# Performance work log

Measured on AMD Instinct MI355X. Metric: run time of the kernel, lower is better.

The kernel has to match this reference:

```python
import jax, jax.numpy as jnp
import numpy as np

D_MODEL = 1024
D_STATE = 16
EXPAND = 2
D_CONV = 4
D_INNER = EXPAND * D_MODEL          # 2048
DT_RANK = D_MODEL // 16             # 64
B = 2
L = 1024
EPS = 1e-5


def setup_inputs() -> dict:
    key = jax.random.key(0)
    ks = jax.random.split(key, 8)
    s = 0.02
    return {
        "x": jax.random.normal(ks[0], (B, L, D_MODEL), jnp.float32),
        "ln_gamma": jnp.ones((D_MODEL,), jnp.float32),
        "ln_beta": jnp.zeros((D_MODEL,), jnp.float32),
        "in_proj_w": jax.random.normal(ks[1], (2 * D_INNER, D_MODEL), jnp.float32) * s,
        "conv_w": jax.random.normal(ks[2], (D_INNER, 1, D_CONV), jnp.float32) * s,
        "conv_b": jnp.zeros((D_INNER,), jnp.float32),
        "x_proj_w": jax.random.normal(ks[3], (DT_RANK + 2 * D_STATE, D_INNER), jnp.float32) * s,
        "dt_proj_w": jax.random.normal(ks[4], (D_INNER, DT_RANK), jnp.float32) * s,
        "dt_proj_b": jax.random.normal(ks[5], (D_INNER,), jnp.float32) * 0.01,
        "A_log": jnp.log(jnp.tile(jnp.arange(1, D_STATE + 1, dtype=jnp.float32), (D_INNER, 1))),
        "D_skip": jnp.ones((D_INNER,), jnp.float32),
        "out_proj_w": jax.random.normal(ks[6], (D_MODEL, D_INNER), jnp.float32) * s,
    }


def _layernorm(x, g, b):
    mu = jnp.mean(x, axis=-1, keepdims=True)
    var = jnp.mean((x - mu) ** 2, axis=-1, keepdims=True)
    return (x - mu) * jax.lax.rsqrt(var + EPS) * g + b


def _mamba_forward(x, ln_gamma, ln_beta, in_proj_w, conv_w, conv_b,
                   x_proj_w, dt_proj_w, dt_proj_b, A_log, D_skip, out_proj_w):
    residual = x
    xn = _layernorm(x, ln_gamma, ln_beta)

    # in_proj -> split into ssm input u and gate z   (b, l, 2*d_inner)
    xz = jnp.einsum('bld,ed->ble', xn, in_proj_w)
    u, z = jnp.split(xz, 2, axis=-1)

    # causal depthwise conv1d (padding = d_conv-1 on the left, truncated to L)
    uc = jnp.transpose(u, (0, 2, 1))  # (b, d_inner, l)
    uc = jax.lax.conv_general_dilated(
        uc, conv_w, window_strides=(1,), padding=[(D_CONV - 1, 0)],
        feature_group_count=D_INNER,
        dimension_numbers=('NCH', 'OIH', 'NCH'))
    uc = uc + conv_b[None, :, None]
    u = jax.nn.silu(jnp.transpose(uc, (0, 2, 1)))  # (b, l, d_inner)

    # selective SSM
    A = -jnp.exp(A_log)                              # (d_inner, d_state)
    x_dbl = jnp.einsum('bld,ed->ble', u, x_proj_w)   # (b, l, dt_rank+2*n)
    dt, Bm, Cm = jnp.split(x_dbl, [DT_RANK, DT_RANK + D_STATE], axis=-1)
    delta = jax.nn.softplus(jnp.einsum('blr,dr->bld', dt, dt_proj_w) + dt_proj_b)

    def step(h, inputs):
        d_t, B_t, C_t, u_t = inputs            # (b,di) (b,n) (b,n) (b,di)
        dA = jnp.exp(d_t[..., None] * A)       # (b, di, n)
        h = dA * h + (d_t * u_t)[..., None] * B_t[:, None, :]
        y = jnp.einsum('bdn,bn->bd', h, C_t)
        return h, y

    h0 = jnp.zeros((x.shape[0], D_INNER, D_STATE), x.dtype)
    xs = (jnp.moveaxis(delta, 1, 0), jnp.moveaxis(Bm, 1, 0),
          jnp.moveaxis(Cm, 1, 0), jnp.moveaxis(u, 1, 0))
    _, ys = jax.lax.scan(step, h0, xs)
    y = jnp.moveaxis(ys, 0, 1) + u * D_skip     # (b, l, d_inner)

    y = y * jax.nn.silu(z)                      # gated output
    out = jnp.einsum('ble,de->bld', y, out_proj_w)
    # dropout is identity in eval mode
    return out + residual


def reference(x, ln_gamma, ln_beta, in_proj_w, conv_w, conv_b,
              x_proj_w, dt_proj_w, dt_proj_b, A_log, D_skip, out_proj_w):
    return _mamba_forward(x, ln_gamma, ln_beta, in_proj_w, conv_w, conv_b,
                          x_proj_w, dt_proj_w, dt_proj_b, A_log, D_skip, out_proj_w)
```

## Files before the change

### kernel.cpp

```cpp
#include <hip/hip_runtime.h>

#define D_MODEL 1024
#define D_STATE 16
#define D_INNER 2048
#define DT_RANK 64
#define NBATCH 2
#define SEQ_L 1024
#define M_ROWS (NBATCH * SEQ_L)
#define CHUNK 64
#define NCHUNK (SEQ_L / CHUNK)

typedef __bf16 bf16x8 __attribute__((ext_vector_type(8)));
typedef float f32x4 __attribute__((ext_vector_type(4)));
typedef unsigned short u16;
typedef unsigned int u32;
typedef u16 u16x8 __attribute__((ext_vector_type(8)));

__device__ __forceinline__ float bf2f(u16 h) {
    return __uint_as_float(((unsigned)h) << 16);
}
__device__ __forceinline__ u16 f2bf(float f) {
    unsigned u = __float_as_uint(f);
    u += 0x7fff + ((u >> 16) & 1);
    return (u16)(u >> 16);
}

__global__ __launch_bounds__(256) void prep(
    const float* __restrict__ s0, const float* __restrict__ s1,
    const float* __restrict__ s2, const float* __restrict__ s3,
    u16* __restrict__ d0, u16* __restrict__ d1,
    u16* __restrict__ d2, u16* __restrict__ d3,
    const float* __restrict__ x, const float* __restrict__ g,
    const float* __restrict__ b, u16* __restrict__ xn,
    float* __restrict__ xd) {
    int blk = blockIdx.x;
    if (blk < 25856) {
        int idx = blk * 256 + threadIdx.x;
        if (idx < 4194304) {
            d0[idx] = f2bf(s0[idx]);
        } else if (idx < 6291456) {
            int i = idx - 4194304; d1[i] = f2bf(s1[i]);
        } else if (idx < 6488064) {
            int i = idx - 6291456; d2[i] = f2bf(s2[i]);
        } else {
            int i = idx - 6488064; d3[i] = f2bf(s3[i]);
        }
        return;
    }
    if (blk < 26048) {
        int zi = (blk - 25856) * 256 + threadIdx.x;
        ((float4*)xd)[zi] = (float4){0.f, 0.f, 0.f, 0.f};
        return;
    }
    int row = blk - 26048;
    const float4* xr = (const float4*)(x + (size_t)row * D_MODEL);
    float4 v = xr[threadIdx.x];
    float s  = v.x + v.y + v.z + v.w;
    float ss = v.x * v.x + v.y * v.y + v.z * v.z + v.w * v.w;
#pragma unroll
    for (int off = 32; off > 0; off >>= 1) {
        s  += __shfl_down(s,  off, 64);
        ss += __shfl_down(ss, off, 64);
    }
    __shared__ float sh_s[4], sh_ss[4];
    int wid = threadIdx.x >> 6;
    if ((threadIdx.x & 63) == 0) { sh_s[wid] = s; sh_ss[wid] = ss; }
    __syncthreads();
    float mu  = (sh_s[0] + sh_s[1] + sh_s[2] + sh_s[3]) * (1.0f / D_MODEL);
    float var = (sh_ss[0] + sh_ss[1] + sh_ss[2] + sh_ss[3]) * (1.0f / D_MODEL) - mu * mu;
    float rs = rsqrtf(var + 1e-5f);
    int c0 = threadIdx.x * 4;
    float vv[4] = {v.x, v.y, v.z, v.w};
#pragma unroll
    for (int j = 0; j < 4; j++) {
        int c = c0 + j;
        float o = (vv[j] - mu) * rs * g[c] + b[c];
        xn[(size_t)row * D_MODEL + c] = f2bf(o);
    }
}

template <int BM, int BN, int WM, int WN, int MODE>
__global__ __launch_bounds__(256) void gemm_lds(
    const __bf16* __restrict__ A, const __bf16* __restrict__ W,
    int K, int Ksteps, int ldC,
    float* __restrict__ outF, u16* __restrict__ outB) {
    constexpr int WCOLS = BN / (WN * 16);
    __shared__ __bf16 As[BM * 32];
    __shared__ __bf16 Bs[BN * 32];
    int tid  = threadIdx.x;
    int lane = tid & 63;
    int wid  = tid >> 6;
    int l16  = lane & 15;
    int quad = lane >> 4;
    int wr = wid / WCOLS;
    int wc = wid % WCOLS;
    int m0 = blockIdx.y * BM;
    int n0 = blockIdx.x * BN;
    int kbase = blockIdx.z * Ksteps * 32;

    f32x4 acc[WM][WN];
#pragma unroll
    for (int mi = 0; mi < WM; mi++)
#pragma unroll
        for (int nj = 0; nj < WN; nj++)
            acc[mi][nj] = (f32x4){0.f, 0.f, 0.f, 0.f};

    for (int ki = 0; ki < Ksteps; ki++) {
        int k0 = kbase + ki * 32;
        __syncthreads();
#pragma unroll
        for (int i = 0; i < BM / 64; i++) {
            int t   = i * 256 + tid;
            int row = t >> 2;
            int cg  = (t & 3) ^ ((row >> 1) & 3);
            __builtin_amdgcn_global_load_lds(
                (const __attribute__((address_space(1))) u32*)(A + (size_t)(m0 + row) * K + k0 + cg * 8),
                (__attribute__((address_space(3))) u32*)(As + (i * 256 + wid * 64) * 8),
                16, 0, 0);
        }
#pragma unroll
        for (int i = 0; i < BN / 64; i++) {
            int t   = i * 256 + tid;
            int row = t >> 2;
            int cg  = (t & 3) ^ ((row >> 1) & 3);
            __builtin_amdgcn_global_load_lds(
                (const __attribute__((address_space(1))) u32*)(W + (size_t)(n0 + row) * K + k0 + cg * 8),
                (__attribute__((address_space(3))) u32*)(Bs + (i * 256 + wid * 64) * 8),
                16, 0, 0);
        }
        __syncthreads();

        bf16x8 af[WM], bfr[WN];
#pragma unroll
        for (int mi = 0; mi < WM; mi++) {
            int r  = wr * WM * 16 + mi * 16 + l16;
            int cg = quad ^ ((r >> 1) & 3);
            af[mi] = *(const bf16x8*)(As + r * 32 + cg * 8);
        }
#pragma unroll
        for (int nj = 0; nj < WN; nj++) {
            int r  = wc * WN * 16 + nj * 16 + l16;
            int cg = quad ^ ((r >> 1) & 3);
            bfr[nj] = *(const bf16x8*)(Bs + r * 32 + cg * 8);
        }
#pragma unroll
        for (int mi = 0; mi < WM; mi++)
#pragma unroll
            for (int nj = 0; nj < WN; nj++)
                acc[mi][nj] = __builtin_amdgcn_mfma_f32_16x16x32_bf16(
                    af[mi], bfr[nj], acc[mi][nj], 0, 0, 0);
    }

    float* outP = (MODE == 4) ? outF + (size_t)blockIdx.z * M_ROWS * ldC : outF;
#pragma unroll
    for (int mi = 0; mi < WM; mi++) {
#pragma unroll
        for (int nj = 0; nj < WN; nj++) {
            int col = n0 + wc * WN * 16 + nj * 16 + l16;
#pragma unroll
            for (int r = 0; r < 4; r++) {
                int row = m0 + wr * WM * 16 + mi * 16 + quad * 4 + r;
                float v = acc[mi][nj][r];
                if (MODE == 0) {
                    outB[(size_t)row * ldC + col] = f2bf(v);
                } else {
                    outP[(size_t)row * ldC + col] = v;
                }
            }
        }
    }
}

__global__ __launch_bounds__(256) void out_reduce(
    const float* __restrict__ p, const float* __restrict__ x,
    float* __restrict__ out) {
    int idx = blockIdx.x * 256 + threadIdx.x;
    const int N = M_ROWS * D_MODEL;
    float4 a = ((const float4*)p)[idx];
    float4 b = ((const float4*)(p + N))[idx];
    float4 c = ((const float4*)(p + 2 * N))[idx];
    float4 d = ((const float4*)(p + 3 * N))[idx];
    float4 r = ((const float4*)x)[idx];
    float4 o;
    o.x = a.x + b.x + c.x + d.x + r.x;
    o.y = a.y + b.y + c.y + d.y + r.y;
    o.z = a.z + b.z + c.z + d.z + r.z;
    o.w = a.w + b.w + c.w + d.w + r.w;
    ((float4*)out)[idx] = o;
}

__global__ __launch_bounds__(256) void gemm_xp(
    const __bf16* __restrict__ A, const __bf16* __restrict__ W,
    float* __restrict__ outF) {
    const int K = D_INNER, Ksplit = D_INNER / 8, Nw = 96;
    int lane = threadIdx.x & 63;
    int wid  = threadIdx.x >> 6;
    int m0 = blockIdx.y * 64;
    int n0 = blockIdx.x * 64;
    int kc = blockIdx.z;
    int l16  = lane & 15;
    int quad = lane >> 4;
    int mrow = m0 + wid * 16 + l16;

    const __bf16* ap = A + (size_t)mrow * K + kc * Ksplit + quad * 8;
    const __bf16* wp[4];
#pragma unroll
    for (int j = 0; j < 4; j++) {
        int nc = n0 + j * 16 + l16;
        if (nc > Nw - 1) nc = Nw - 1;
        wp[j] = W + (size_t)nc * K + kc * Ksplit + quad * 8;
    }
    f32x4 acc[4];
#pragma unroll
    for (int j = 0; j < 4; j++) acc[j] = (f32x4){0.f, 0.f, 0.f, 0.f};

    for (int k = 0; k < Ksplit; k += 32) {
        bf16x8 a = *(const bf16x8*)ap;
        ap += 32;
#pragma unroll
        for (int j = 0; j < 4; j++) {
            bf16x8 bfr = *(const bf16x8*)wp[j];
            wp[j] += 32;
            acc[j] = __builtin_amdgcn_mfma_f32_16x16x32_bf16(a, bfr, acc[j], 0, 0, 0);
        }
    }
#pragma unroll
    for (int j = 0; j < 4; j++) {
        int col = n0 + j * 16 + l16;
        if (col < Nw) {
#pragma unroll
            for (int r = 0; r < 4; r++) {
                int row = m0 + wid * 16 + quad * 4 + r;
                atomicAdd(outF + (size_t)row * 96 + col, acc[j][r]);
            }
        }
    }
}

__global__ __launch_bounds__(256) void gemm_dt(
    const float* __restrict__ A, const __bf16* __restrict__ W,
    const float* __restrict__ bias, u16* __restrict__ outB16) {
    int lane = threadIdx.x & 63;
    int wid  = threadIdx.x >> 6;
    int m0 = blockIdx.y * 64;
    int n0 = blockIdx.x * 64;
    int l16  = lane & 15;
    int quad = lane >> 4;
    int mrow = m0 + wid * 16 + l16;

    const float* ap = A + (size_t)mrow * 96 + quad * 8;
    const __bf16* wp[4];
#pragma unroll
    for (int j = 0; j < 4; j++) {
        int nc = n0 + j * 16 + l16;
        wp[j] = W + (size_t)nc * DT_RANK + quad * 8;
    }
    f32x4 acc[4];
#pragma unroll
    for (int j = 0; j < 4; j++) acc[j] = (f32x4){0.f, 0.f, 0.f, 0.f};

#pragma unroll
    for (int k = 0; k < DT_RANK; k += 32) {
        float4 v0 = *(const float4*)(ap);
        float4 v1 = *(const float4*)(ap + 4);
        ap += 32;
        u16x8 pk;
        pk[0] = f2bf(v0.x); pk[1] = f2bf(v0.y); pk[2] = f2bf(v0.z); pk[3] = f2bf(v0.w);
        pk[4] = f2bf(v1.x); pk[5] = f2bf(v1.y); pk[6] = f2bf(v1.z); pk[7] = f2bf(v1.w);
        bf16x8 a = __builtin_bit_cast(bf16x8, pk);
#pragma unroll
        for (int j = 0; j < 4; j++) {
            bf16x8 bfr = *(const bf16x8*)wp[j];
            wp[j] += 32;
            acc[j] = __builtin_amdgcn_mfma_f32_16x16x32_bf16(a, bfr, acc[j], 0, 0, 0);
        }
    }
#pragma unroll
    for (int j = 0; j < 4; j++) {
        int col = n0 + j * 16 + l16;
#pragma unroll
        for (int r = 0; r < 4; r++) {
            int row = m0 + wid * 16 + quad * 4 + r;
            float t = acc[j][r] + bias[col];
            float sp = (t > 20.f) ? t : log1pf(__expf(t));
            outB16[(size_t)row * D_INNER + col] = f2bf(sp);
        }
    }
}

__global__ __launch_bounds__(256) void conv_silu(
    const u16* __restrict__ xz, const float* __restrict__ cw,
    const float* __restrict__ cb, u16* __restrict__ uc) {
    int idx = blockIdx.x * 256 + threadIdx.x;
    int d = idx & (D_INNER - 1);
    int m = idx >> 11;
    int t = m & (SEQ_L - 1);
    float s = cb[d];
#pragma unroll
    for (int j = 0; j < 4; j++) {
        int tt = t - 3 + j;
        if (tt >= 0) {
            s += cw[d * 4 + j] *
                 bf2f(xz[(size_t)(m - 3 + j) * (2 * D_INNER) + d]);
        }
    }
    float sig = 1.f / (1.f + __expf(-s));
    uc[idx] = f2bf(s * sig);
}

__global__ __launch_bounds__(256) void scan_chunk(
    const u16* __restrict__ delta, const u16* __restrict__ uc,
    const float* __restrict__ xd, const float* __restrict__ A_log,
    float* __restrict__ Pst, float* __restrict__ Sst) {
    __shared__ float Bsh[CHUNK][16];
    int tid  = threadIdx.x;
    int lane = tid & 63;
    int w    = tid >> 6;
    int dsub = lane & 15;
    int g    = lane >> 4;
    int n0   = g * 4;
    int c = blockIdx.x, b = blockIdx.z;
    int d = blockIdx.y * 64 + w * 16 + dsub;
    int mbase = b * SEQ_L + c * CHUNK;

    {
        int row = tid >> 2, q = tid & 3;
        *(float4*)&Bsh[row][q * 4] =
            *(const float4*)(xd + (size_t)(mbase + row) * 96 + DT_RANK + q * 4);
    }
    __syncthreads();

    float a[4];
    {
        float4 a0 = *(const float4*)(A_log + d * D_STATE + n0);
        a[0] = -__expf(a0.x); a[1] = -__expf(a0.y);
        a[2] = -__expf(a0.z); a[3] = -__expf(a0.w);
    }
    float P[4] = {1.f, 1.f, 1.f, 1.f}, S[4] = {0.f, 0.f, 0.f, 0.f};

    for (int t0 = 0; t0 < CHUNK; t0 += 4) {
        float dlv[4], uv[4];
#pragma unroll
        for (int i = 0; i < 4; i++) {
            int m = mbase + t0 + i;
            dlv[i] = bf2f(delta[(size_t)m * D_INNER + d]);
            uv[i]  = bf2f(uc[(size_t)m * D_INNER + d]);
        }
#pragma unroll
        for (int i = 0; i < 4; i++) {
            float c1 = dlv[i] * uv[i];
#pragma unroll
            for (int j = 0; j < 4; j++) {
                float dA = __expf(dlv[i] * a[j]);
                P[j] *= dA;
                S[j] = dA * S[j] + c1 * Bsh[t0 + i][n0 + j];
            }
        }
    }
    size_t s = ((size_t)(b * D_INNER + d) * NCHUNK + c) * D_STATE + n0;
    *(float4*)(Pst + s) = (float4){P[0], P[1], P[2], P[3]};
    *(float4*)(Sst + s) = (float4){S[0], S[1], S[2], S[3]};
}

__global__ __launch_bounds__(256) void scan_apply(
    const u16* __restrict__ delta, const u16* __restrict__ uc,
    const float* __restrict__ xd, const u16* __restrict__ xz,
    const float* __restrict__ A_log, const float* __restrict__ Dsk,
    const float* __restrict__ Pst, const float* __restrict__ Sst,
    u16* __restrict__ yg) {
    __shared__ float BCs[CHUNK][32];
    int tid  = threadIdx.x;
    int lane = tid & 63;
    int w    = tid >> 6;
    int dsub = lane & 15;
    int g    = lane >> 4;
    int n0   = g * 4;
    int c = blockIdx.x, b = blockIdx.z;
    int d = blockIdx.y * 64 + w * 16 + dsub;
    int mbase = b * SEQ_L + c * CHUNK;

    {
#pragma unroll
        for (int i = 0; i < 2; i++) {
            int idx = i * 256 + tid;
            int row = idx >> 3, q = idx & 7;
            *(float4*)&BCs[row][q * 4] =
                *(const float4*)(xd + (size_t)(mbase + row) * 96 + DT_RANK + q * 4);
        }
    }

    float h[4] = {0.f, 0.f, 0.f, 0.f};
    {
        size_t base = ((size_t)(b * D_INNER + d) * NCHUNK) * D_STATE + n0;
        for (int cc = 0; cc < c; cc++) {
            float4 Pv = *(const float4*)(Pst + base + (size_t)cc * D_STATE);
            float4 Sv = *(const float4*)(Sst + base + (size_t)cc * D_STATE);
            h[0] = Pv.x * h[0] + Sv.x;
            h[1] = Pv.y * h[1] + Sv.y;
            h[2] = Pv.z * h[2] + Sv.z;
            h[3] = Pv.w * h[3] + Sv.w;
        }
    }

    float a[4];
    {
        float4 a0 = *(const float4*)(A_log + d * D_STATE + n0);
        a[0] = -__expf(a0.x); a[1] = -__expf(a0.y);
        a[2] = -__expf(a0.z); a[3] = -__expf(a0.w);
    }
    float dsk = Dsk[d];
    __syncthreads();

    for (int t0 = 0; t0 < CHUNK; t0 += 4) {
        float dlv[4], uv[4], zv[4];
#pragma unroll
        for (int i = 0; i < 4; i++) {
            int m = mbase + t0 + i;
            dlv[i] = bf2f(delta[(size_t)m * D_INNER + d]);
            uv[i]  = bf2f(uc[(size_t)m * D_INNER + d]);
            zv[i]  = bf2f(xz[(size_t)m * (2 * D_INNER) + D_INNER + d]);
        }
#pragma unroll
        for (int i = 0; i < 4; i++) {
            int t = t0 + i;
            float c1 = dlv[i] * uv[i];
            float y = 0.f;
#pragma unroll
            for (int j = 0; j < 4; j++) {
                float dA = __expf(dlv[i] * a[j]);
                h[j] = dA * h[j] + c1 * BCs[t][n0 + j];
                y += h[j] * BCs[t][16 + n0 + j];
            }
            y += __shfl_xor(y, 16);
            y += __shfl_xor(y, 32);
            if (g == 0) {
                float z = zv[i];
                float yv = y + uv[i] * dsk;
                float gt = z / (1.f + __expf(-z));
                yg[(size_t)(mbase + t) * D_INNER + d] = f2bf(yv * gt);
            }
        }
    }
}

extern "C" void kernel_launch(void* const* d_in, const int* in_sizes, int n_in,
                              void* d_out, int out_size, void* d_ws, size_t ws_size,
                              hipStream_t stream) {
    const float* x         = (const float*)d_in[0];
    const float* ln_g      = (const float*)d_in[1];
    const float* ln_b      = (const float*)d_in[2];
    const float* in_proj_w = (const float*)d_in[3];
    const float* conv_w    = (const float*)d_in[4];
    const float* conv_b    = (const float*)d_in[5];
    const float* x_proj_w  = (const float*)d_in[6];
    const float* dt_proj_w = (const float*)d_in[7];
    const float* dt_proj_b = (const float*)d_in[8];
    const float* A_log     = (const float*)d_in[9];
    const float* Dsk       = (const float*)d_in[10];
    const float* out_proj_w= (const float*)d_in[11];

    char* ws = (char*)d_ws;
    u16* xn   = (u16*)ws;    ws += (size_t)M_ROWS * D_MODEL * 2;
    u16* xz   = (u16*)ws;    ws += (size_t)M_ROWS * 2 * D_INNER * 2;
    u16* ucv  = (u16*)ws;    ws += (size_t)M_ROWS * D_INNER * 2;
    float* xd = (float*)ws;  ws += (size_t)M_ROWS * 96 * 4;
    u16* dl   = (u16*)ws;    ws += (size_t)M_ROWS * D_INNER * 2;
    u16* yg   = (u16*)ws;    ws += (size_t)M_ROWS * D_INNER * 2;
    u16* w_in = (u16*)ws;    ws += (size_t)4194304 * 2;
    u16* w_out= (u16*)ws;    ws += (size_t)2097152 * 2;
    u16* w_xp = (u16*)ws;    ws += (size_t)196608 * 2;
    u16* w_dt = (u16*)ws;    ws += (size_t)131072 * 2;
    float* Pst = (float*)ws; ws += (size_t)NBATCH * D_INNER * D_STATE * NCHUNK * 4;
    float* Sst = (float*)ws; ws += (size_t)NBATCH * D_INNER * D_STATE * NCHUNK * 4;
    float* opart = (float*)ws;

    prep<<<26048 + M_ROWS, 256, 0, stream>>>(
        in_proj_w, out_proj_w, x_proj_w, dt_proj_w, w_in, w_out, w_xp, w_dt,
        x, ln_g, ln_b, xn, xd);
    gemm_lds<64, 128, 4, 2, 0><<<dim3(4096 / 128, M_ROWS / 64, 1), 256, 0, stream>>>(
        (const __bf16*)xn, (const __bf16*)w_in, D_MODEL, D_MODEL / 32, 2 * D_INNER,
        nullptr, xz);
    conv_silu<<<(M_ROWS * D_INNER) / 256, 256, 0, stream>>>(xz, conv_w, conv_b, ucv);
    gemm_xp<<<dim3(2, 32, 8), 256, 0, stream>>>(
        (const __bf16*)ucv, (const __bf16*)w_xp, xd);
    gemm_dt<<<dim3(32, 32, 1), 256, 0, stream>>>(
        xd, (const __bf16*)w_dt, dt_proj_b, dl);
    dim3 sgrid(NCHUNK, D_INNER / 64, NBATCH);
    scan_chunk<<<sgrid, 256, 0, stream>>>(dl, ucv, xd, A_log, Pst, Sst);
    scan_apply<<<sgrid, 256, 0, stream>>>(dl, ucv, xd, xz, A_log, Dsk, Pst, Sst, yg);
    gemm_lds<64, 128, 4, 2, 4><<<dim3(1024 / 128, M_ROWS / 64, 4), 256, 0, stream>>>(
        (const __bf16*)yg, (const __bf16*)w_out, D_INNER, D_INNER / 4 / 32, D_MODEL,
        opart, nullptr);
    out_reduce<<<(M_ROWS * D_MODEL / 4) / 256, 256, 0, stream>>>(
        opart, x, (float*)d_out);
}
```

Before: 278.2 us.

## Fuse chunked scan passes into one kernel with inter-block flag handoff

Merges the chunk-summary and apply passes of the selective scan into one kernel. Each block writes its chunk's (P,S) state and publishes a release flag, then spins on the flags of earlier chunks before combining prefix states. The block also stages delta, u and z tiles in LDS once, so the second pass does not re-read them from global memory. The chunk size is halved to give more blocks, and prep zeroes the flag array. In exchange it depends on co-residency and forward-progress ordering of the spinning blocks, which risks stalls or deadlock if earlier chunks are not scheduled first.

After: 477.9 us. 1.72x slower.

```diff
diff --git a/kernel.cpp b/kernel.cpp
--- a/kernel.cpp
+++ b/kernel.cpp
@@ -7,7 +7,7 @@
 #define NBATCH 2
 #define SEQ_L 1024
 #define M_ROWS (NBATCH * SEQ_L)
-#define CHUNK 64
+#define CHUNK 32
 #define NCHUNK (SEQ_L / CHUNK)
 
 typedef __bf16 bf16x8 __attribute__((ext_vector_type(8)));
@@ -47,12 +47,12 @@
         }
         return;
     }
-    if (blk < 26048) {
+    if (blk < 26050) {
         int zi = (blk - 25856) * 256 + threadIdx.x;
         ((float4*)xd)[zi] = (float4){0.f, 0.f, 0.f, 0.f};
         return;
     }
-    int row = blk - 26048;
+    int row = blk - 26050;
     const float4* xr = (const float4*)(x + (size_t)row * D_MODEL);
     float4 v = xr[threadIdx.x];
     float s  = v.x + v.y + v.z + v.w;
@@ -308,11 +308,16 @@
     uc[idx] = f2bf(s * sig);
 }
 
-__global__ __launch_bounds__(256) void scan_chunk(
+__global__ __launch_bounds__(256, 8) void scan_fused(
     const u16* __restrict__ delta, const u16* __restrict__ uc,
-    const float* __restrict__ xd, const float* __restrict__ A_log,
-    float* __restrict__ Pst, float* __restrict__ Sst) {
-    __shared__ float Bsh[CHUNK][16];
+    const float* __restrict__ xd, const u16* __restrict__ xz,
+    const float* __restrict__ A_log, const float* __restrict__ Dsk,
+    float* __restrict__ Pst, float* __restrict__ Sst,
+    u32* __restrict__ flags, u16* __restrict__ yg) {
+    __shared__ float BCs[CHUNK][32];
+    __shared__ u16 DLs[CHUNK][64];
+    __shared__ u16 UCs[CHUNK][64];
+    __shared__ u16 Zs[CHUNK][64];
     int tid  = threadIdx.x;
     int lane = tid & 63;
     int w    = tid >> 6;
@@ -320,13 +325,21 @@
     int g    = lane >> 4;
     int n0   = g * 4;
     int c = blockIdx.x, b = blockIdx.z;
-    int d = blockIdx.y * 64 + w * 16 + dsub;
+    int d0 = blockIdx.y * 64;
+    int dloc = w * 16 + dsub;
+    int d = d0 + dloc;
     int mbase = b * SEQ_L + c * CHUNK;
+    u32* fl = flags + (b * 32 + blockIdx.y) * NCHUNK;
 
     {
-        int row = tid >> 2, q = tid & 3;
-        *(float4*)&Bsh[row][q * 4] =
-            *(const float4*)(xd + (size_t)(mbase + row) * 96 + DT_RANK + q * 4);
+        int r = tid >> 3, c8 = (tid & 7) * 8, q = tid & 7;
+        size_t gb = (size_t)(mbase + r) * D_INNER + d0 + c8;
+        *(u16x8*)&DLs[r][c8] = *(const u16x8*)(delta + gb);
+        *(u16x8*)&UCs[r][c8] = *(const u16x8*)(uc + gb);
+        *(u16x8*)&Zs[r][c8]  = *(const u16x8*)(
+            xz + (size_t)(mbase + r) * (2 * D_INNER) + D_INNER + d0 + c8);
+        *(float4*)&BCs[r][q * 4] =
+            *(const float4*)(xd + (size_t)(mbase + r) * 96 + DT_RANK + q * 4);
     }
     __syncthreads();
 
@@ -336,15 +349,15 @@
         a[0] = -__expf(a0.x); a[1] = -__expf(a0.y);
         a[2] = -__expf(a0.z); a[3] = -__expf(a0.w);
     }
+    float dsk = Dsk[d];
+
     float P[4] = {1.f, 1.f, 1.f, 1.f}, S[4] = {0.f, 0.f, 0.f, 0.f};
-
     for (int t0 = 0; t0 < CHUNK; t0 += 4) {
         float dlv[4], uv[4];
 #pragma unroll
         for (int i = 0; i < 4; i++) {
-            int m = mbase + t0 + i;
-            dlv[i] = bf2f(delta[(size_t)m * D_INNER + d]);
-            uv[i]  = bf2f(uc[(size_t)m * D_INNER + d]);
+            dlv[i] = bf2f(DLs[t0 + i][dloc]);
+            uv[i]  = bf2f(UCs[t0 + i][dloc]);
         }
 #pragma unroll
         for (int i = 0; i < 4; i++) {
@@ -353,44 +366,29 @@
             for (int j = 0; j < 4; j++) {
                 float dA = __expf(dlv[i] * a[j]);
                 P[j] *= dA;
-                S[j] = dA * S[j] + c1 * Bsh[t0 + i][n0 + j];
-            }
-        }
-    }
-    size_t s = ((size_t)(b * D_INNER + d) * NCHUNK + c) * D_STATE + n0;
-    *(float4*)(Pst + s) = (float4){P[0], P[1], P[2], P[3]};
-    *(float4*)(Sst + s) = (float4){S[0], S[1], S[2], S[3]};
-}
-
-__global__ __launch_bounds__(256) void scan_apply(
-    const u16* __restrict__ delta, const u16* __restrict__ uc,
-    const float* __restrict__ xd, const u16* __restrict__ xz,
-    const float* __restrict__ A_log, const float* __restrict__ Dsk,
-    const float* __restrict__ Pst, const float* __restrict__ Sst,
-    u16* __restrict__ yg) {
-    __shared__ float BCs[CHUNK][32];
-    int tid  = threadIdx.x;
-    int lane = tid & 63;
-    int w    = tid >> 6;
-    int dsub = lane & 15;
-    int g    = lane >> 4;
-    int n0   = g * 4;
-    int c = blockIdx.x, b = blockIdx.z;
-    int d = blockIdx.y * 64 + w * 16 + dsub;
-    int mbase = b * SEQ_L + c * CHUNK;
-
-    {
-#pragma unroll
-        for (int i = 0; i < 2; i++) {
-            int idx = i * 256 + tid;
-            int row = idx >> 3, q = idx & 7;
-            *(float4*)&BCs[row][q * 4] =
-                *(const float4*)(xd + (size_t)(mbase + row) * 96 + DT_RANK + q * 4);
-        }
+                S[j] = dA * S[j] + c1 * BCs[t0 + i][n0 + j];
+            }
+        }
+    }
+    size_t sidx = ((size_t)(b * D_INNER + d) * NCHUNK + c) * D_STATE + n0;
+    *(float4*)(Pst + sidx) = (float4){P[0], P[1], P[2], P[3]};
+    *(float4*)(Sst + sidx) = (float4){S[0], S[1], S[2], S[3]};
+    __syncthreads();
+    if (tid == 0) {
+        __threadfence();
+        __hip_atomic_store(&fl[c], 1u, __ATOMIC_RELEASE, __HIP_MEMORY_SCOPE_AGENT);
     }
 
     float h[4] = {0.f, 0.f, 0.f, 0.f};
-    {
+    if (c > 0) {
+        if (tid < c) {
+            while (__hip_atomic_load(&fl[tid], __ATOMIC_ACQUIRE,
+                                     __HIP_MEMORY_SCOPE_AGENT) == 0u) {
+                __builtin_amdgcn_s_sleep(1);
+            }
+            __threadfence();
+        }
+        __syncthreads();
         size_t base = ((size_t)(b * D_INNER + d) * NCHUNK) * D_STATE + n0;
         for (int cc = 0; cc < c; cc++) {
             float4 Pv = *(const float4*)(Pst + base + (size_t)cc * D_STATE);
@@ -402,23 +400,13 @@
         }
     }
 
-    float a[4];
-    {
-        float4 a0 = *(const float4*)(A_log + d * D_STATE + n0);
-        a[0] = -__expf(a0.x); a[1] = -__expf(a0.y);
-        a[2] = -__expf(a0.z); a[3] = -__expf(a0.w);
-    }
-    float dsk = Dsk[d];
-    __syncthreads();
-
     for (int t0 = 0; t0 < CHUNK; t0 += 4) {
         float dlv[4], uv[4], zv[4];
 #pragma unroll
         for (int i = 0; i < 4; i++) {
-            int m = mbase + t0 + i;
-            dlv[i] = bf2f(delta[(size_t)m * D_INNER + d]);
-            uv[i]  = bf2f(uc[(size_t)m * D_INNER + d]);
-            zv[i]  = bf2f(xz[(size_t)m * (2 * D_INNER) + D_INNER + d]);
+            dlv[i] = bf2f(DLs[t0 + i][dloc]);
+            uv[i]  = bf2f(UCs[t0 + i][dloc]);
+            zv[i]  = bf2f(Zs[t0 + i][dloc]);
         }
 #pragma unroll
         for (int i = 0; i < 4; i++) {
@@ -464,6 +452,7 @@
     u16* xz   = (u16*)ws;    ws += (size_t)M_ROWS * 2 * D_INNER * 2;
     u16* ucv  = (u16*)ws;    ws += (size_t)M_ROWS * D_INNER * 2;
     float* xd = (float*)ws;  ws += (size_t)M_ROWS * 96 * 4;
+    u32* flags= (u32*)ws;    ws += (size_t)2048 * 4;
     u16* dl   = (u16*)ws;    ws += (size_t)M_ROWS * D_INNER * 2;
     u16* yg   = (u16*)ws;    ws += (size_t)M_ROWS * D_INNER * 2;
     u16* w_in = (u16*)ws;    ws += (size_t)4194304 * 2;
@@ -474,7 +463,7 @@
     float* Sst = (float*)ws; ws += (size_t)NBATCH * D_INNER * D_STATE * NCHUNK * 4;
     float* opart = (float*)ws;
 
-    prep<<<26048 + M_ROWS, 256, 0, stream>>>(
+    prep<<<26050 + M_ROWS, 256, 0, stream>>>(
         in_proj_w, out_proj_w, x_proj_w, dt_proj_w, w_in, w_out, w_xp, w_dt,
         x, ln_g, ln_b, xn, xd);
     gemm_lds<64, 128, 4, 2, 0><<<dim3(4096 / 128, M_ROWS / 64, 1), 256, 0, stream>>>(
@@ -485,9 +474,8 @@
         (const __bf16*)ucv, (const __bf16*)w_xp, xd);
     gemm_dt<<<dim3(32, 32, 1), 256, 0, stream>>>(
         xd, (const __bf16*)w_dt, dt_proj_b, dl);
-    dim3 sgrid(NCHUNK, D_INNER / 64, NBATCH);
-    scan_chunk<<<sgrid, 256, 0, stream>>>(dl, ucv, xd, A_log, Pst, Sst);
-    scan_apply<<<sgrid, 256, 0, stream>>>(dl, ucv, xd, xz, A_log, Dsk, Pst, Sst, yg);
+    scan_fused<<<dim3(NCHUNK, D_INNER / 64, NBATCH), 256, 0, stream>>>(
+        dl, ucv, xd, xz, A_log, Dsk, Pst, Sst, flags, yg);
     gemm_lds<64, 128, 4, 2, 4><<<dim3(1024 / 128, M_ROWS / 64, 4), 256, 0, stream>>>(
         (const __bf16*)yg, (const __bf16*)w_out, D_INNER, D_INNER / 4 / 32, D_MODEL,
         opart, nullptr);
```
